# Kernel tuning notes

Hardware: AMD Instinct MI355X
Metric: run time of the kernel (lower is better)

Reference implementation:

```python
import jax, jax.numpy as jnp
import numpy as np

D_MODEL = 1024
NUM_HEADS = 16
D_KEY = D_MODEL // NUM_HEADS
MASK_FUTURE = True
NEG_INF = -jnp.inf


def setup_inputs() -> dict:
    key = jax.random.key(0)
    ks = jax.random.split(key, 7)
    B, N = 4, 2048
    return {
        "query": jax.random.normal(ks[0], (B, N, D_MODEL), dtype=jnp.float32),
        "key": jax.random.normal(ks[1], (B, N, D_MODEL), dtype=jnp.float32),
        "value": jax.random.normal(ks[2], (B, N, D_MODEL), dtype=jnp.float32),
        "mask": jnp.ones((B, N), dtype=jnp.int32),
        "Wq": jax.random.normal(ks[3], (D_MODEL, D_MODEL), dtype=jnp.float32) * 0.02,
        "Wk": jax.random.normal(ks[4], (D_MODEL, D_MODEL), dtype=jnp.float32) * 0.02,
        "Wv": jax.random.normal(ks[5], (D_MODEL, D_MODEL), dtype=jnp.float32) * 0.02,
        "Wo": jax.random.normal(ks[6], (D_MODEL, D_MODEL), dtype=jnp.float32) * 0.02,
    }


def reference(query, key, value, mask, Wq, Wk, Wv, Wo):
    B, Nq, _ = query.shape
    Nk = key.shape[1]
    # Linear projections (bias=False), split into heads: [B, H, N, d_key]
    def proj(x, W, N):
        return (x @ W).reshape(B, N, NUM_HEADS, D_KEY).transpose(0, 2, 1, 3)
    Q = proj(query, Wq, Nq)
    K = proj(key, Wk, Nk)
    V = proj(value, Wv, Nk)
    # Scaled dot-product scores: [B, H, Nq, Nk]
    scores = jnp.einsum("bhqd,bhkd->bhqk", Q, K) / np.sqrt(D_KEY).astype(np.float32)
    # Padding mask: mask [B, Nk] == 0 -> -inf (broadcast over heads and query dim)
    scores = jnp.where(mask[:, None, None, :] == 0, NEG_INF, scores)
    if MASK_FUTURE:
        causal = jnp.triu(jnp.ones((Nq, Nk), dtype=jnp.bool_), k=1)
        scores = jnp.where(causal[None, None, :, :], NEG_INF, scores)
    attn = jax.nn.softmax(scores, axis=-1)
    out = jnp.einsum("bhqk,bhkd->bhqd", attn, V)  # [B, H, Nq, d_key]
    out = out.transpose(0, 2, 1, 3).reshape(B, Nq, D_MODEL)
    return out @ Wo
```

## Files before the change

kernel.cpp:

```cpp
#include <hip/hip_runtime.h>
#include <hip/hip_bf16.h>

typedef unsigned short u16;
typedef unsigned int u32;
typedef short s16x8 __attribute__((ext_vector_type(8)));
typedef float f32x4 __attribute__((ext_vector_type(4)));
typedef float f32x16 __attribute__((ext_vector_type(16)));
typedef u16 u16x4 __attribute__((ext_vector_type(4)));
typedef u32 u32x4 __attribute__((ext_vector_type(4)));

#define D_MODEL 1024
#define NHEAD 16
#define DK 64
#define B_ 4
#define N_ 2048
#define M_TOT (B_ * N_)
#define QBLK 128
#define KVBLK 64
#define SCALE2 0.1803368801111137f
#define FRAG_PER_BH 131072
#define EX2(x) __builtin_amdgcn_exp2f(x)

__device__ __forceinline__ u16 f2b(float x) {
  __hip_bfloat16 h = __float2bfloat16(x);
  return __builtin_bit_cast(u16, h);
}

__device__ __forceinline__ u32 cvtpk(float lo, float hi) {
  u32 r;
  asm("v_cvt_pk_bf16_f32 %0, %1, %2" : "=v"(r) : "v"(lo), "v"(hi));
  return r;
}

__device__ __forceinline__ void gload_lds16(const void* gp, void* lp) {
  __builtin_amdgcn_global_load_lds(
      (const __attribute__((address_space(1))) unsigned int*)gp,
      (__attribute__((address_space(3))) unsigned int*)lp, 16, 0, 0);
}

__global__ __launch_bounds__(256) void cvt3_f32_bf16(const float* __restrict__ x0,
                                                     const float* __restrict__ x1,
                                                     const float* __restrict__ x2,
                                                     u16* __restrict__ y0,
                                                     u16* __restrict__ y1,
                                                     u16* __restrict__ y2, int n4) {
  int z = blockIdx.y;
  const float* x = z == 0 ? x0 : (z == 1 ? x1 : x2);
  u16* y = z == 0 ? y0 : (z == 1 ? y1 : y2);
  int i = blockIdx.x * 256 + threadIdx.x;
  if (i < n4) {
    f32x4 v = *(const f32x4*)(x + (size_t)i * 4);
    u16x4 o;
    o[0] = f2b(v[0]); o[1] = f2b(v[1]); o[2] = f2b(v[2]); o[3] = f2b(v[3]);
    *(u16x4*)(y + (size_t)i * 4) = o;
  }
}

__global__ __launch_bounds__(256) void mask_bias(const int* __restrict__ mask,
                                                 float* __restrict__ Mb, int n) {
  int i = blockIdx.x * 256 + threadIdx.x;
  if (i < n) Mb[i] = mask[i] ? 0.f : -INFINITY;
}

__global__ __launch_bounds__(256) void wtrans4(const float* __restrict__ W0,
                                               const float* __restrict__ W1,
                                               const float* __restrict__ W2,
                                               const float* __restrict__ W3,
                                               u16* __restrict__ T0,
                                               u16* __restrict__ T1,
                                               u16* __restrict__ T2,
                                               u16* __restrict__ T3) {
  __shared__ float tile[32][33];
  int z = blockIdx.z;
  const float* W = z == 0 ? W0 : (z == 1 ? W1 : (z == 2 ? W2 : W3));
  u16* Wt = z == 0 ? T0 : (z == 1 ? T1 : (z == 2 ? T2 : T3));
  int bi = blockIdx.y, bj = blockIdx.x;
  int tx = threadIdx.x & 31, ty = threadIdx.x >> 5;
#pragma unroll
  for (int r = 0; r < 4; ++r)
    tile[ty + r * 8][tx] = W[(size_t)(bi * 32 + ty + r * 8) * D_MODEL + bj * 32 + tx];
  __syncthreads();
#pragma unroll
  for (int r = 0; r < 4; ++r)
    Wt[(size_t)(bj * 32 + ty + r * 8) * D_MODEL + bi * 32 + tx] = f2b(tile[tx][ty + r * 8]);
}

template <int MODE>
__device__ __forceinline__ void gemm_body(const u16* __restrict__ A,
                                          const u16* __restrict__ Bt,
                                          float* __restrict__ Cf,
                                          u16* __restrict__ Cb) {
  const int N = D_MODEL, K = D_MODEL;
  __shared__ __align__(16) u16 Atile[128 * 32];
  __shared__ __align__(16) u16 Btile[128 * 32];
  int tid = threadIdx.x;
  int w = tid >> 6, lane = tid & 63;
  int g = lane >> 4, c = lane & 15;
  int wr = w >> 1, wc = w & 1;
  int bid = blockIdx.x;
  int xcd = bid & 7, idx = bid >> 3;
  int bi = xcd * 8 + (idx & 7);
  int bj = idx >> 3;
  const int rowA0 = bi * 128, rowB0 = bj * 128;

  const f32x4 fzero = {0.f, 0.f, 0.f, 0.f};
  f32x4 acc[4][4];
#pragma unroll
  for (int m = 0; m < 4; ++m)
#pragma unroll
    for (int n = 0; n < 4; ++n) acc[m][n] = fzero;

  for (int k0 = 0; k0 < K; k0 += 32) {
#pragma unroll
    for (int cc = 0; cc < 2; ++cc) {
      int li = w * 2 + cc;
      const u16* ga = A + (size_t)(rowA0 + li * 16 + (lane >> 2)) * K + k0 + (lane & 3) * 8;
      gload_lds16(ga, &Atile[li * 512]);
      const u16* gb = Bt + (size_t)(rowB0 + li * 16 + (lane >> 2)) * K + k0 + (lane & 3) * 8;
      gload_lds16(gb, &Btile[li * 512]);
    }
    __syncthreads();
    s16x8 af[4], bfr[4];
#pragma unroll
    for (int m = 0; m < 4; ++m)
      af[m] = *(const s16x8*)&Atile[(wr * 64 + m * 16 + c) * 32 + g * 8];
#pragma unroll
    for (int n = 0; n < 4; ++n)
      bfr[n] = *(const s16x8*)&Btile[(wc * 64 + n * 16 + c) * 32 + g * 8];
#pragma unroll
    for (int m = 0; m < 4; ++m)
#pragma unroll
      for (int n = 0; n < 4; ++n)
        acc[m][n] = __builtin_amdgcn_mfma_f32_16x16x32_bf16(af[m], bfr[n], acc[m][n], 0, 0, 0);
    __syncthreads();
  }

  if (MODE == 0) {
#pragma unroll
    for (int m = 0; m < 4; ++m)
#pragma unroll
      for (int n = 0; n < 4; ++n)
#pragma unroll
        for (int r = 0; r < 4; ++r) {
          int row = rowA0 + wr * 64 + m * 16 + g * 4 + r;
          int col = rowB0 + wc * 64 + n * 16 + c;
          Cf[(size_t)row * N + col] = acc[m][n][r];
        }
  } else if (MODE == 1) {
    int bb = rowA0 >> 11;
    int hloc = bj * 2 + wc;
    size_t fb = ((size_t)bb * NHEAD + hloc) * FRAG_PER_BH;
#pragma unroll
    for (int m = 0; m < 4; ++m) {
      int rowm = rowA0 + wr * 64 + m * 16;
      size_t f32b = (size_t)((rowm & 2047) >> 5) * 4;
      int lpart = (m & 1) * 16 + g * 4 + (c >> 3) * 32;
#pragma unroll
      for (int n = 0; n < 4; ++n)
#pragma unroll
        for (int r = 0; r < 4; ++r)
          Cb[fb + (f32b + n) * 512 + (size_t)(lpart + r) * 8 + (c & 7)] = f2b(acc[m][n][r]);
    }
  } else {
    int bb = rowA0 >> 11;
    int hloc = bj * 2 + wc;
    size_t fb = ((size_t)bb * NHEAD + hloc) * FRAG_PER_BH;
#pragma unroll
    for (int m = 0; m < 4; ++m) {
      int rowm = rowA0 + wr * 64 + m * 16;
      size_t kv16b = (size_t)((rowm & 2047) >> 4) * 2;
#pragma unroll
      for (int n = 0; n < 4; ++n) {
        size_t idxo = fb + (kv16b + (n >> 1)) * 512 +
                      (size_t)((n & 1) * 16 + c + (g >> 1) * 32) * 8 + (g & 1) * 4;
        u16x4 pv;
        pv[0] = f2b(acc[m][n][0]); pv[1] = f2b(acc[m][n][1]);
        pv[2] = f2b(acc[m][n][2]); pv[3] = f2b(acc[m][n][3]);
        *(u16x4*)&Cb[idxo] = pv;
      }
    }
  }
}

__global__ __launch_bounds__(256) void gemm_kfrag(const u16* __restrict__ A,
                                                  const u16* __restrict__ Bt,
                                                  u16* __restrict__ C) {
  gemm_body<1>(A, Bt, nullptr, C);
}

__global__ __launch_bounds__(256) void gemm_vfrag(const u16* __restrict__ A,
                                                  const u16* __restrict__ Bt,
                                                  u16* __restrict__ C) {
  gemm_body<2>(A, Bt, nullptr, C);
}

__global__ __launch_bounds__(256) void gemm_f32(const u16* __restrict__ A,
                                                const u16* __restrict__ Bt,
                                                float* __restrict__ C) {
  gemm_body<0>(A, Bt, C, nullptr);
}

#define MAX4(a, b, c, d) fmaxf(fmaxf(a, b), fmaxf(c, d))

__global__ __launch_bounds__(256) void attn_fwd(const u16* __restrict__ Qf,
                                                const u16* __restrict__ Kf,
                                                const u16* __restrict__ Vf,
                                                const float* __restrict__ Mb,
                                                u16* __restrict__ Out) {
  int bid = blockIdx.x;
  int xcd = bid & 7;
  int inner = bid >> 3;
  int j = inner >> 3;
  int pair = inner & 7;
  int bh = xcd * 8 + j;
  int b = bh >> 4, h = bh & 15;
  int tid = threadIdx.x, w = tid >> 6, lane = tid & 63;
  int q32 = lane & 31, hi = lane >> 5;
  int hi4 = hi * 4;

  const u16* qfb0 = Qf + (size_t)(b * NHEAD + h) * FRAG_PER_BH + lane * 8;
  const u16* kfb0 = Kf + (size_t)(b * NHEAD + h) * FRAG_PER_BH + lane * 8;
  const u16* vfb0 = Vf + (size_t)(b * NHEAD + h) * FRAG_PER_BH + lane * 8;
  const float* mb0 = Mb + (size_t)b * N_ + hi4;

  const f32x16 fz16 = {0.f, 0.f, 0.f, 0.f, 0.f, 0.f, 0.f, 0.f,
                       0.f, 0.f, 0.f, 0.f, 0.f, 0.f, 0.f, 0.f};

#pragma unroll 1
  for (int ph = 0; ph < 2; ++ph) {
    int qt = ph ? pair : 15 - pair;
    int q0 = qt * QBLK;
    int wq0 = q0 + w * 32;
    int ntw = wq0 / KVBLK + 1;
    int qq = wq0 + q32;

    const u16* kfp = kfb0;
    const u16* vfp = vfb0;
    const float* mpl = mb0;

    s16x8 qf[4];
#pragma unroll
    for (int kk = 0; kk < 4; ++kk)
      qf[kk] = *(const s16x8*)(qfb0 + ((size_t)((wq0 >> 5) * 4 + kk)) * 512);

    f32x16 oacc[2];
    oacc[0] = fz16; oacc[1] = fz16;
    float mr = -1e30f, lr = 0.f;

    auto loadk = [&](s16x8(&kf)[2][4], const u16* kp) {
#pragma unroll
      for (int n = 0; n < 2; ++n)
#pragma unroll
        for (int kk = 0; kk < 4; ++kk)
          kf[n][kk] = *(const s16x8*)(kp + (n * 4 + kk) * 512);
    };

    auto step = [&](s16x8(&kc)[2][4], s16x8(&kn)[2][4], int t) {
      int kv0 = t * KVBLK;
      s16x8 vf[2][2][2];
#pragma unroll
      for (int n = 0; n < 2; ++n)
#pragma unroll
        for (int kk2 = 0; kk2 < 2; ++kk2)
#pragma unroll
          for (int d0 = 0; d0 < 2; ++d0)
            vf[n][kk2][d0] = *(const s16x8*)(vfp + ((n * 2 + kk2) * 2 + d0) * 512);
      f32x4 mbv[2][4];
#pragma unroll
      for (int n = 0; n < 2; ++n)
#pragma unroll
        for (int jj = 0; jj < 4; ++jj)
          mbv[n][jj] = *(const f32x4*)(mpl + n * 32 + jj * 8);
      if (t + 1 < ntw) loadk(kn, kfp + 4096);

      f32x16 st[2];
#pragma unroll
      for (int n = 0; n < 2; ++n) {
        f32x16 a = fz16;
        a = __builtin_amdgcn_mfma_f32_32x32x16_bf16(kc[n][0], qf[0], a, 0, 0, 0);
        a = __builtin_amdgcn_mfma_f32_32x32x16_bf16(kc[n][1], qf[1], a, 0, 0, 0);
        a = __builtin_amdgcn_mfma_f32_32x32x16_bf16(kc[n][2], qf[2], a, 0, 0, 0);
        a = __builtin_amdgcn_mfma_f32_32x32x16_bf16(kc[n][3], qf[3], a, 0, 0, 0);
        st[n] = a;
      }

      bool diag = (kv0 + KVBLK - 1 > wq0);
#pragma unroll
      for (int n = 0; n < 2; ++n)
#pragma unroll
        for (int r = 0; r < 16; ++r) {
          float v = fmaf(st[n][r], SCALE2, mbv[n][r >> 2][r & 3]);
          if (diag) {
            int kv = kv0 + n * 32 + (r & 3) + 8 * (r >> 2) + hi4;
            v = (kv > qq) ? -INFINITY : v;
          }
          st[n][r] = v;
        }
      float a0 = MAX4(st[0][0], st[0][1], st[0][2], st[0][3]);
      float a1 = MAX4(st[0][4], st[0][5], st[0][6], st[0][7]);
      float a2 = MAX4(st[0][8], st[0][9], st[0][10], st[0][11]);
      float a3 = MAX4(st[0][12], st[0][13], st[0][14], st[0][15]);
      float b0 = MAX4(st[1][0], st[1][1], st[1][2], st[1][3]);
      float b1 = MAX4(st[1][4], st[1][5], st[1][6], st[1][7]);
      float b2 = MAX4(st[1][8], st[1][9], st[1][10], st[1][11]);
      float b3 = MAX4(st[1][12], st[1][13], st[1][14], st[1][15]);
      float pmax = fmaxf(MAX4(a0, a1, a2, a3), MAX4(b0, b1, b2, b3));

      if (__any(pmax > mr + 8.f)) {
        float pm2 = fmaxf(pmax, __shfl_xor(pmax, 32));
        float mnew = fmaxf(mr, pm2);
        float al = EX2(mr - mnew);
        mr = mnew;
        lr *= al;
#pragma unroll
        for (int r = 0; r < 16; ++r) {
          float alT = __shfl(al, (r & 3) + 8 * (r >> 2) + hi4);
          oacc[0][r] *= alT;
          oacc[1][r] *= alT;
        }
      }

      s16x8 pa[2][2];
#pragma unroll
      for (int n = 0; n < 2; ++n) {
#pragma unroll
        for (int r = 0; r < 16; ++r) st[n][r] = EX2(st[n][r] - mr);
        float s01 = st[n][0] + st[n][1], s23 = st[n][2] + st[n][3];
        float s45 = st[n][4] + st[n][5], s67 = st[n][6] + st[n][7];
        float s89 = st[n][8] + st[n][9], sab = st[n][10] + st[n][11];
        float scd = st[n][12] + st[n][13], sef = st[n][14] + st[n][15];
        lr += ((s01 + s23) + (s45 + s67)) + ((s89 + sab) + (scd + sef));
        u32 x0 = cvtpk(st[n][0], st[n][1]);
        u32 x1 = cvtpk(st[n][2], st[n][3]);
        u32 x2 = cvtpk(st[n][4], st[n][5]);
        u32 x3 = cvtpk(st[n][6], st[n][7]);
        auto sA = __builtin_amdgcn_permlane32_swap(x0, x2, false, false);
        auto sB = __builtin_amdgcn_permlane32_swap(x1, x3, false, false);
        u32x4 w0 = {sA[0], sB[0], sA[1], sB[1]};
        pa[n][0] = __builtin_bit_cast(s16x8, w0);
        u32 x4 = cvtpk(st[n][8], st[n][9]);
        u32 x5 = cvtpk(st[n][10], st[n][11]);
        u32 x6 = cvtpk(st[n][12], st[n][13]);
        u32 x7 = cvtpk(st[n][14], st[n][15]);
        auto sC = __builtin_amdgcn_permlane32_swap(x4, x6, false, false);
        auto sD = __builtin_amdgcn_permlane32_swap(x5, x7, false, false);
        u32x4 w1 = {sC[0], sD[0], sC[1], sD[1]};
        pa[n][1] = __builtin_bit_cast(s16x8, w1);
      }

#pragma unroll
      for (int n = 0; n < 2; ++n)
#pragma unroll
        for (int kk2 = 0; kk2 < 2; ++kk2)
#pragma unroll
          for (int d0 = 0; d0 < 2; ++d0)
            oacc[d0] = __builtin_amdgcn_mfma_f32_32x32x16_bf16(pa[n][kk2], vf[n][kk2][d0], oacc[d0], 0, 0, 0);

      kfp += 4096;
      vfp += 4096;
      mpl += KVBLK;
    };

    s16x8 kA[2][4], kB[2][4];
    loadk(kA, kfp);
    for (int t = 0; t < ntw; t += 2) {
      step(kA, kB, t);
      if (t + 1 < ntw) step(kB, kA, t + 1);
    }

    lr += __shfl_xor(lr, 32);
#pragma unroll
    for (int r = 0; r < 16; ++r) {
      int qoff = (r & 3) + 8 * (r >> 2) + hi4;
      float lq = __shfl(lr, qoff);
      float inv = lq > 0.f ? 1.f / lq : 0.f;
      size_t base = (size_t)(b * N_ + wq0 + qoff) * D_MODEL + h * DK + q32;
      Out[base] = f2b(oacc[0][r] * inv);
      Out[base + 32] = f2b(oacc[1][r] * inv);
    }
  }
}

extern "C" void kernel_launch(void* const* d_in, const int* in_sizes, int n_in,
                              void* d_out, int out_size, void* d_ws, size_t ws_size,
                              hipStream_t stream) {
  const float* q = (const float*)d_in[0];
  const float* k = (const float*)d_in[1];
  const float* v = (const float*)d_in[2];
  const int* mask = (const int*)d_in[3];
  const float* Wq = (const float*)d_in[4];
  const float* Wk = (const float*)d_in[5];
  const float* Wv = (const float*)d_in[6];
  const float* Wo = (const float*)d_in[7];
  float* out = (float*)d_out;

  char* ws = (char*)d_ws;
  const size_t SZ = (size_t)M_TOT * D_MODEL * 2;
  u16* qb = (u16*)ws;
  u16* kb = (u16*)(ws + SZ);
  u16* vb = (u16*)(ws + 2 * SZ);
  u16* Qf = (u16*)(ws + 3 * SZ);
  u16* Vf = (u16*)(ws + 4 * SZ);
  u16* Wqt = (u16*)(ws + 5 * SZ);
  u16* Wkt = Wqt + 1024 * 1024;
  u16* Wvt = Wkt + 1024 * 1024;
  u16* Wot = Wvt + 1024 * 1024;
  float* Mb = (float*)(Wot + 1024 * 1024);
  u16* Kf = qb;
  u16* attn_out = kb;

  int n4 = M_TOT * D_MODEL / 4;
  cvt3_f32_bf16<<<dim3(n4 / 256, 3), 256, 0, stream>>>(q, k, v, qb, kb, vb, n4);
  mask_bias<<<(B_ * N_ + 255) / 256, 256, 0, stream>>>(mask, Mb, B_ * N_);
  wtrans4<<<dim3(32, 32, 4), 256, 0, stream>>>(Wq, Wk, Wv, Wo, Wqt, Wkt, Wvt, Wot);
  gemm_kfrag<<<512, 256, 0, stream>>>(qb, Wqt, Qf);
  gemm_kfrag<<<512, 256, 0, stream>>>(kb, Wkt, Kf);
  gemm_vfrag<<<512, 256, 0, stream>>>(vb, Wvt, Vf);
  attn_fwd<<<512, 256, 0, stream>>>(Qf, Kf, Vf, Mb, attn_out);
  gemm_f32<<<512, 256, 0, stream>>>(attn_out, Wot, out);
}
```

Before: 245.1 us.

## Batch QKV projections into one launch and split attention into single-wave blocks

Merges the three projection GEMMs into one grid-z launch, so the Q, K and V work share a single wave of blocks and avoid two launch tails. K output gets its own workspace region, since the merged launch would otherwise overwrite qb while it is still being read. The attention kernel now runs one 64-thread wave per block (2048 blocks) instead of four waves per 256-thread block. This lets causal-imbalanced waves retire independently and improves scheduling flexibility, at the cost of any intra-block sharing and a larger workspace footprint.

New measurement: 226.9 us. -7.4%, faster.

```diff
diff --git a/kernel.cpp b/kernel.cpp
--- a/kernel.cpp
+++ b/kernel.cpp
@@ -182,16 +182,19 @@
   }
 }
 
-__global__ __launch_bounds__(256) void gemm_kfrag(const u16* __restrict__ A,
-                                                  const u16* __restrict__ Bt,
-                                                  u16* __restrict__ C) {
-  gemm_body<1>(A, Bt, nullptr, C);
-}
-
-__global__ __launch_bounds__(256) void gemm_vfrag(const u16* __restrict__ A,
-                                                  const u16* __restrict__ Bt,
-                                                  u16* __restrict__ C) {
-  gemm_body<2>(A, Bt, nullptr, C);
+__global__ __launch_bounds__(256) void gemm_qkv(const u16* __restrict__ Aq,
+                                                const u16* __restrict__ Ak,
+                                                const u16* __restrict__ Av,
+                                                const u16* __restrict__ Btq,
+                                                const u16* __restrict__ Btk,
+                                                const u16* __restrict__ Btv,
+                                                u16* __restrict__ Cq,
+                                                u16* __restrict__ Ck,
+                                                u16* __restrict__ Cv) {
+  int z = blockIdx.y;
+  if (z == 0) gemm_body<1>(Aq, Btq, nullptr, Cq);
+  else if (z == 1) gemm_body<1>(Ak, Btk, nullptr, Ck);
+  else gemm_body<2>(Av, Btv, nullptr, Cv);
 }
 
 __global__ __launch_bounds__(256) void gemm_f32(const u16* __restrict__ A,
@@ -202,19 +205,21 @@
 
 #define MAX4(a, b, c, d) fmaxf(fmaxf(a, b), fmaxf(c, d))
 
-__global__ __launch_bounds__(256) void attn_fwd(const u16* __restrict__ Qf,
-                                                const u16* __restrict__ Kf,
-                                                const u16* __restrict__ Vf,
-                                                const float* __restrict__ Mb,
-                                                u16* __restrict__ Out) {
+__global__ __launch_bounds__(64) void attn_fwd(const u16* __restrict__ Qf,
+                                               const u16* __restrict__ Kf,
+                                               const u16* __restrict__ Vf,
+                                               const float* __restrict__ Mb,
+                                               u16* __restrict__ Out) {
   int bid = blockIdx.x;
   int xcd = bid & 7;
   int inner = bid >> 3;
-  int j = inner >> 3;
-  int pair = inner & 7;
+  int j = inner >> 5;
+  int u = inner & 31;
+  int pair = u >> 2;
+  int w = u & 3;
   int bh = xcd * 8 + j;
   int b = bh >> 4, h = bh & 15;
-  int tid = threadIdx.x, w = tid >> 6, lane = tid & 63;
+  int lane = threadIdx.x & 63;
   int q32 = lane & 31, hi = lane >> 5;
   int hi4 = hi * 4;
 
@@ -407,15 +412,14 @@
   u16* Wot = Wvt + 1024 * 1024;
   float* Mb = (float*)(Wot + 1024 * 1024);
   u16* Kf = qb;
+  Kf = (u16*)(ws + 5 * SZ + 4 * 2 * 1024 * 1024 + ((B_ * N_ * 4 + 255) & ~255));
   u16* attn_out = kb;
 
   int n4 = M_TOT * D_MODEL / 4;
   cvt3_f32_bf16<<<dim3(n4 / 256, 3), 256, 0, stream>>>(q, k, v, qb, kb, vb, n4);
   mask_bias<<<(B_ * N_ + 255) / 256, 256, 0, stream>>>(mask, Mb, B_ * N_);
   wtrans4<<<dim3(32, 32, 4), 256, 0, stream>>>(Wq, Wk, Wv, Wo, Wqt, Wkt, Wvt, Wot);
-  gemm_kfrag<<<512, 256, 0, stream>>>(qb, Wqt, Qf);
-  gemm_kfrag<<<512, 256, 0, stream>>>(kb, Wkt, Kf);
-  gemm_vfrag<<<512, 256, 0, stream>>>(vb, Wvt, Vf);
-  attn_fwd<<<512, 256, 0, stream>>>(Qf, Kf, Vf, Mb, attn_out);
+  gemm_qkv<<<dim3(512, 3), 256, 0, stream>>>(qb, kb, vb, Wqt, Wkt, Wvt, Qf, Kf, Vf);
+  attn_fwd<<<2048, 64, 0, stream>>>(Qf, Kf, Vf, Mb, attn_out);
   gemm_f32<<<512, 256, 0, stream>>>(attn_out, Wot, out);
 }
```
